# Optimization experiments

Hardware: AMD Instinct MI355X
Metric: run time of the kernel (lower is better)

Reference implementation:

```python
import jax, jax.numpy as jnp
import numpy as np

N, E, G = 50000, 800000, 64
IN, HID, HEADS, OUT = 128, 64, 4, 128
NEG = 0.2  # PyG GATConv default negative_slope


def setup_inputs() -> dict:
    key = jax.random.key(0)
    ks = jax.random.split(key, 12)
    nrm = lambda k, shape, s: (jax.random.normal(k, shape, jnp.float32) * s)
    x = nrm(ks[0], (N, IN), 1.0)
    edge_index = jax.random.randint(ks[1], (2, E), 0, N)
    batch = jnp.sort(jax.random.randint(ks[2], (N,), 0, G))
    W1 = nrm(ks[3], (IN, HEADS * HID), IN ** -0.5)
    a1_src = nrm(ks[4], (HEADS, HID), HID ** -0.5)
    a1_dst = nrm(ks[5], (HEADS, HID), HID ** -0.5)
    b1 = jnp.zeros((HEADS * HID,), jnp.float32)
    W2 = nrm(ks[6], (HEADS * HID, OUT), (HEADS * HID) ** -0.5)
    a2_src = nrm(ks[7], (1, OUT), OUT ** -0.5)
    a2_dst = nrm(ks[8], (1, OUT), OUT ** -0.5)
    b2 = jnp.zeros((OUT,), jnp.float32)
    fc_W = nrm(ks[9], (OUT, OUT), OUT ** -0.5)
    fc_b = jnp.zeros((OUT,), jnp.float32)
    return dict(x=x, edge_index=edge_index, batch=batch, W1=W1, a1_src=a1_src,
                a1_dst=a1_dst, b1=b1, W2=W2, a2_src=a2_src, a2_dst=a2_dst,
                b2=b2, fc_W=fc_W, fc_b=fc_b)


def gat_conv(x, W, a_src, a_dst, b, src, dst, heads):
    n = x.shape[0]
    ch = W.shape[1] // heads
    h = (x @ W).reshape(n, heads, ch)                      # [n, H, C]
    al_s = jnp.einsum('nhc,hc->nh', h, a_src)              # per-node src logits
    al_d = jnp.einsum('nhc,hc->nh', h, a_dst)
    e = al_s[src] + al_d[dst]                              # [E, H]
    e = jnp.where(e > 0, e, NEG * e)                       # LeakyReLU
    # segment softmax over incoming edges of each dst node
    m = jax.lax.stop_gradient(jax.ops.segment_max(e, dst, num_segments=n))
    m = jnp.where(jnp.isfinite(m), m, 0.0)
    ex = jnp.exp(e - m[dst])
    s = jax.ops.segment_sum(ex, dst, num_segments=n)
    alpha = ex / (s[dst] + 1e-16)                          # [E, H]
    out = jax.ops.segment_sum(h[src] * alpha[..., None], dst, num_segments=n)
    return out.reshape(n, heads * ch) + b                  # concat heads + bias


def reference(x, edge_index, batch, W1, a1_src, a1_dst, b1, W2, a2_src, a2_dst, b2, fc_W, fc_b):
    loops = jnp.arange(N, dtype=edge_index.dtype)          # PyG adds self-loops
    src = jnp.concatenate([edge_index[0], loops])
    dst = jnp.concatenate([edge_index[1], loops])
    h = jax.nn.elu(gat_conv(x, W1, a1_src, a1_dst, b1, src, dst, HEADS))
    h = jax.nn.elu(gat_conv(h, W2, a2_src, a2_dst, b2, src, dst, 1))
    sums = jax.ops.segment_sum(h, batch, num_segments=G)
    cnt = jax.ops.segment_sum(jnp.ones((N,), h.dtype), batch, num_segments=G)
    pooled = sums / jnp.maximum(cnt, 1.0)[:, None]         # global mean pool
    return jax.nn.relu(pooled @ fc_W + fc_b)
```

## Files before the change

kernel.cpp:

```cpp
#include <hip/hip_runtime.h>
#include <math.h>

#define N_NODES 50000
#define N_EDGES 800000
#define N_GRAPHS 64
#define NEG 0.2f
#define CTS 132

typedef unsigned short us;
typedef us us2 __attribute__((ext_vector_type(2)));
typedef us us4 __attribute__((ext_vector_type(4)));
typedef us us8 __attribute__((ext_vector_type(8)));
typedef short bf16x8 __attribute__((ext_vector_type(8)));
typedef float f32x4 __attribute__((ext_vector_type(4)));

__device__ __forceinline__ us bf16rn(float f) {
  unsigned int u = __float_as_uint(f);
  u += 0x7FFFu + ((u >> 16) & 1u);
  return (us)(u >> 16);
}
__device__ __forceinline__ float bf2f(us h) {
  return __uint_as_float(((unsigned int)h) << 16);
}
__device__ __forceinline__ float readlane_f(float v, int l) {
  return __uint_as_float((unsigned)__builtin_amdgcn_readlane(__float_as_uint(v), l));
}

__global__ __launch_bounds__(256) void prep_kernel(
    const float* __restrict__ x, us* __restrict__ xh, us* __restrict__ xl,
    const float* __restrict__ W1, const float* __restrict__ W2,
    us* __restrict__ w1h, us* __restrict__ w1l,
    us* __restrict__ w2h, us* __restrict__ w2l,
    int* __restrict__ cnt, float* __restrict__ psum) {
  int bid = blockIdx.x, t = threadIdx.x;
  if (bid < 6250) {
    int i = bid * 256 + t;
    float4 v = *(const float4*)&x[(size_t)i * 4];
    us h0 = bf16rn(v.x), h1 = bf16rn(v.y), h2 = bf16rn(v.z), h3 = bf16rn(v.w);
    us4 hv = {h0, h1, h2, h3};
    us4 lv = {bf16rn(v.x - bf2f(h0)), bf16rn(v.y - bf2f(h1)),
              bf16rn(v.z - bf2f(h2)), bf16rn(v.w - bf2f(h3))};
    *(us4*)&xh[(size_t)i * 4] = hv;
    *(us4*)&xl[(size_t)i * 4] = lv;
  } else if (bid < 6506) {
    int idx = (bid - 6250) * 256 + t;
    const float* W; us *oh, *ol; int K, N, li;
    if (idx < 128 * 256) { W = W1; oh = w1h; ol = w1l; K = 128; N = 256; li = idx; }
    else { W = W2; oh = w2h; ol = w2l; K = 256; N = 128; li = idx - 128 * 256; }
    int n = li / K, k = li - n * K;
    float f = W[(size_t)k * N + n];
    us h = bf16rn(f);
    oh[li] = h;
    ol[li] = bf16rn(f - bf2f(h));
  } else {
    int i = (bid - 6506) * 256 + t;
    if (i < N_NODES) cnt[i] = 0;
    if (i < N_GRAPHS * 128) psum[i] = 0.f;
  }
}

__global__ __launch_bounds__(256, 2) void gemm_bf16x3(
    const us* __restrict__ Agh, const us* __restrict__ Agl,
    const us* __restrict__ Bth, const us* __restrict__ Btl,
    us* __restrict__ C, int M, int N, int K, int heads,
    const float* __restrict__ a_src, const float* __restrict__ a_dst,
    float* __restrict__ al_s, float* __restrict__ al_d) {
  __shared__ us smem[4][128][40];
  int t = threadIdx.x;
  int m0 = blockIdx.x * 128;
  int n0 = blockIdx.y * 128;
  int w = t >> 6, l = t & 63;
  int wr = w >> 1, wc = w & 1;
  int l15 = l & 15, g = l >> 4;

  f32x4 acc[4][4] = {};

  for (int kb = 0; kb < K; kb += 32) {
    us8 z = {};
    #pragma unroll
    for (int i = 0; i < 2; i++) {
      int slot = i * 256 + t;
      int row = slot >> 2, kq = slot & 3;
      size_t gi = (size_t)(m0 + row) * K + kb + kq * 8;
      bool ok = (m0 + row) < M;
      *(us8*)&smem[0][row][kq * 8] = ok ? *(const us8*)&Agh[gi] : z;
      *(us8*)&smem[1][row][kq * 8] = ok ? *(const us8*)&Agl[gi] : z;
    }
    #pragma unroll
    for (int i = 0; i < 2; i++) {
      int slot = i * 256 + t;
      int n = slot >> 2, kq = slot & 3;
      size_t gi = (size_t)(n0 + n) * K + kb + kq * 8;
      *(us8*)&smem[2][n][kq * 8] = *(const us8*)&Bth[gi];
      *(us8*)&smem[3][n][kq * 8] = *(const us8*)&Btl[gi];
    }
    __syncthreads();

    bf16x8 af[4], al4[4], bf[4], bl4[4];
    #pragma unroll
    for (int i = 0; i < 4; i++) {
      af[i]  = *(const bf16x8*)&smem[0][wr * 64 + i * 16 + l15][g * 8];
      al4[i] = *(const bf16x8*)&smem[1][wr * 64 + i * 16 + l15][g * 8];
      bf[i]  = *(const bf16x8*)&smem[2][wc * 64 + i * 16 + l15][g * 8];
      bl4[i] = *(const bf16x8*)&smem[3][wc * 64 + i * 16 + l15][g * 8];
    }
    #pragma unroll
    for (int i = 0; i < 4; i++)
      #pragma unroll
      for (int j = 0; j < 4; j++) {
        acc[i][j] = __builtin_amdgcn_mfma_f32_16x16x32_bf16(af[i], bf[j], acc[i][j], 0, 0, 0);
        acc[i][j] = __builtin_amdgcn_mfma_f32_16x16x32_bf16(af[i], bl4[j], acc[i][j], 0, 0, 0);
        acc[i][j] = __builtin_amdgcn_mfma_f32_16x16x32_bf16(al4[i], bf[j], acc[i][j], 0, 0, 0);
      }
    __syncthreads();
  }

  us* ct = &smem[0][0][0];
  #pragma unroll
  for (int i = 0; i < 4; i++)
    #pragma unroll
    for (int j = 0; j < 4; j++)
      #pragma unroll
      for (int r = 0; r < 4; r++) {
        int row = wr * 64 + i * 16 + g * 4 + r;
        int col = wc * 64 + j * 16 + l15;
        ct[row * CTS + col] = bf16rn(acc[i][j][r]);
      }
  __syncthreads();
  #pragma unroll
  for (int q = 0; q < 8; q++) {
    int slot = q * 256 + t;
    int row = slot >> 4, col8 = slot & 15;
    if (m0 + row < M) {
      us8 v = *(const us8*)&ct[row * CTS + col8 * 8];
      *(us8*)&C[(size_t)(m0 + row) * N + n0 + col8 * 8] = v;
    }
  }

  if (heads == 4) {
    int r = t & 127, hs = t >> 7;
    int row = m0 + r;
    if (row < M) {
      int head = blockIdx.y * 2 + hs;
      const float* as = &a_src[head * 64];
      const float* ad = &a_dst[head * 64];
      float ss = 0.f, sd = 0.f;
      #pragma unroll
      for (int k8 = 0; k8 < 8; k8++) {
        us8 v = *(const us8*)&ct[r * CTS + hs * 64 + k8 * 8];
        #pragma unroll
        for (int j = 0; j < 8; j++) {
          float f = bf2f(v[j]);
          ss += f * as[k8 * 8 + j];
          sd += f * ad[k8 * 8 + j];
        }
      }
      al_s[row * 4 + head] = ss;
      al_d[row * 4 + head] = sd;
    }
  } else if (heads == 1) {
    if (t < 128) {
      int row = m0 + t;
      if (row < M) {
        float ss = 0.f, sd = 0.f;
        #pragma unroll
        for (int k8 = 0; k8 < 16; k8++) {
          us8 v = *(const us8*)&ct[t * CTS + k8 * 8];
          #pragma unroll
          for (int j = 0; j < 8; j++) {
            float f = bf2f(v[j]);
            ss += f * a_src[k8 * 8 + j];
            sd += f * a_dst[k8 * 8 + j];
          }
        }
        al_s[row] = ss;
        al_d[row] = sd;
      }
    }
  }
}

__global__ __launch_bounds__(256) void count_kernel(const int* __restrict__ dst,
                                                    int* __restrict__ cnt) {
  int e = blockIdx.x * 256 + threadIdx.x;
  if (e < N_EDGES) atomicAdd(&cnt[dst[e]], 1);
}

__global__ __launch_bounds__(256) void scan1_kernel(const int* __restrict__ cnt,
                                                    int* __restrict__ itmp,
                                                    int* __restrict__ bsum) {
  int i = blockIdx.x * 256 + threadIdx.x;
  int v = (i < N_NODES) ? cnt[i] : 0;
  int lane = threadIdx.x & 63, w = threadIdx.x >> 6;
  int s = v;
  #pragma unroll
  for (int off = 1; off < 64; off <<= 1) {
    int tv = __shfl_up(s, off);
    if (lane >= off) s += tv;
  }
  __shared__ int wsum[4];
  if (lane == 63) wsum[w] = s;
  __syncthreads();
  int add = 0;
  for (int p = 0; p < w; p++) add += wsum[p];
  s += add;
  if (i < N_NODES) itmp[i] = s;
  if (threadIdx.x == 255) bsum[blockIdx.x] = s;
}

__global__ __launch_bounds__(256) void scan3_kernel(const int* __restrict__ cnt,
                                                    const int* __restrict__ itmp,
                                                    const int* __restrict__ bsum,
                                                    int* __restrict__ rowst,
                                                    int* __restrict__ cursor,
                                                    int nb) {
  int t = threadIdx.x;
  int lane = t & 63, w = t >> 6;
  int v = (t < nb && t < blockIdx.x) ? bsum[t] : 0;
  int s = v;
  #pragma unroll
  for (int off = 1; off < 64; off <<= 1) s += __shfl_xor(s, off);
  __shared__ int partial[4];
  if (lane == 0) partial[w] = s;
  __syncthreads();
  int boff = partial[0] + partial[1] + partial[2] + partial[3];
  int i = blockIdx.x * 256 + t;
  if (i < N_NODES) {
    int excl = itmp[i] - cnt[i] + boff;
    rowst[i] = excl;
    cursor[i] = excl;
  }
  if (i == 0) rowst[N_NODES] = N_EDGES;
}

__global__ __launch_bounds__(256) void scatter_kernel(
    const int* __restrict__ src, const int* __restrict__ dst,
    int* __restrict__ cursor, int* __restrict__ csr_src) {
  int e = blockIdx.x * 256 + threadIdx.x;
  if (e < N_EDGES) {
    int p = atomicAdd(&cursor[dst[e]], 1);
    csr_src[p] = src[e];
  }
}

__global__ __launch_bounds__(256) void agg1_kernel(
    const us* __restrict__ h1b, const float* __restrict__ al_s,
    const float* __restrict__ al_d, const int* __restrict__ rowst,
    const int* __restrict__ csrc, const float* __restrict__ b1,
    us* __restrict__ outh, us* __restrict__ outl) {
  int d = (blockIdx.x * 256 + threadIdx.x) >> 6;
  int lane = threadIdx.x & 63;
  if (d >= N_NODES) return;
  int head = lane >> 4;
  int c0 = lane * 4;
  int wsel = lane & 48;
  float ald = al_d[d * 4 + head];
  float wsum = 0.f, a0 = 0.f, a1 = 0.f, a2 = 0.f, a3 = 0.f;
  {
    float v = al_s[d * 4 + head] + ald;
    v = v > 0.f ? v : NEG * v;
    float w = __expf(v);
    us4 hv = *(const us4*)&h1b[(size_t)d * 256 + c0];
    wsum += w;
    a0 += w * bf2f(hv[0]); a1 += w * bf2f(hv[1]);
    a2 += w * bf2f(hv[2]); a3 += w * bf2f(hv[3]);
  }
  int beg = rowst[d], end = rowst[d + 1];
  int j = beg;
  for (; j + 16 <= end; j += 16) {
    int el = lane & 15;
    int sv = csrc[j + el];
    float v = al_s[sv * 4 + head] + ald;
    v = v > 0.f ? v : NEG * v;
    float wv = __expf(v);
    #pragma unroll
    for (int q = 0; q < 16; q += 4) {
      int s0 = __builtin_amdgcn_readlane(sv, q + 0);
      int s1 = __builtin_amdgcn_readlane(sv, q + 1);
      int s2 = __builtin_amdgcn_readlane(sv, q + 2);
      int s3 = __builtin_amdgcn_readlane(sv, q + 3);
      us4 h0 = *(const us4*)&h1b[(size_t)(unsigned)s0 * 256 + c0];
      us4 h1 = *(const us4*)&h1b[(size_t)(unsigned)s1 * 256 + c0];
      us4 h2 = *(const us4*)&h1b[(size_t)(unsigned)s2 * 256 + c0];
      us4 h3 = *(const us4*)&h1b[(size_t)(unsigned)s3 * 256 + c0];
      float w0 = __shfl(wv, q + 0 + wsel);
      float w1 = __shfl(wv, q + 1 + wsel);
      float w2 = __shfl(wv, q + 2 + wsel);
      float w3 = __shfl(wv, q + 3 + wsel);
      wsum += w0 + w1 + w2 + w3;
      a0 += w0 * bf2f(h0[0]) + w1 * bf2f(h1[0]) + w2 * bf2f(h2[0]) + w3 * bf2f(h3[0]);
      a1 += w0 * bf2f(h0[1]) + w1 * bf2f(h1[1]) + w2 * bf2f(h2[1]) + w3 * bf2f(h3[1]);
      a2 += w0 * bf2f(h0[2]) + w1 * bf2f(h1[2]) + w2 * bf2f(h2[2]) + w3 * bf2f(h3[2]);
      a3 += w0 * bf2f(h0[3]) + w1 * bf2f(h1[3]) + w2 * bf2f(h2[3]) + w3 * bf2f(h3[3]);
    }
  }
  int m = end - j;
  if (m > 0) {
    int el = lane & 15;
    int sv = csrc[j + (el < m ? el : 0)];
    float v = al_s[sv * 4 + head] + ald;
    v = v > 0.f ? v : NEG * v;
    float wv = __expf(v);
    for (int q = 0; q < m; q += 4) {
      int k0 = q, k1 = q + 1 < m ? q + 1 : 0, k2 = q + 2 < m ? q + 2 : 0,
          k3 = q + 3 < m ? q + 3 : 0;
      int s0 = __builtin_amdgcn_readlane(sv, k0);
      int s1 = __builtin_amdgcn_readlane(sv, k1);
      int s2 = __builtin_amdgcn_readlane(sv, k2);
      int s3 = __builtin_amdgcn_readlane(sv, k3);
      us4 h0 = *(const us4*)&h1b[(size_t)(unsigned)s0 * 256 + c0];
      us4 h1 = *(const us4*)&h1b[(size_t)(unsigned)s1 * 256 + c0];
      us4 h2 = *(const us4*)&h1b[(size_t)(unsigned)s2 * 256 + c0];
      us4 h3 = *(const us4*)&h1b[(size_t)(unsigned)s3 * 256 + c0];
      float w0 = __shfl(wv, k0 + wsel);
      float w1 = __shfl(wv, k1 + wsel);
      float w2 = __shfl(wv, k2 + wsel);
      float w3 = __shfl(wv, k3 + wsel);
      if (q + 1 >= m) w1 = 0.f;
      if (q + 2 >= m) w2 = 0.f;
      if (q + 3 >= m) w3 = 0.f;
      wsum += w0 + w1 + w2 + w3;
      a0 += w0 * bf2f(h0[0]) + w1 * bf2f(h1[0]) + w2 * bf2f(h2[0]) + w3 * bf2f(h3[0]);
      a1 += w0 * bf2f(h0[1]) + w1 * bf2f(h1[1]) + w2 * bf2f(h2[1]) + w3 * bf2f(h3[1]);
      a2 += w0 * bf2f(h0[2]) + w1 * bf2f(h1[2]) + w2 * bf2f(h2[2]) + w3 * bf2f(h3[2]);
      a3 += w0 * bf2f(h0[3]) + w1 * bf2f(h1[3]) + w2 * bf2f(h2[3]) + w3 * bf2f(h3[3]);
    }
  }
  float inv = 1.f / (wsum + 1e-16f);
  float4 bb = *(const float4*)&b1[c0];
  float o[4] = {a0 * inv + bb.x, a1 * inv + bb.y, a2 * inv + bb.z, a3 * inv + bb.w};
  us4 oh, ol;
  #pragma unroll
  for (int i = 0; i < 4; i++) {
    float e = o[i] > 0.f ? o[i] : expm1f(o[i]);
    us h = bf16rn(e);
    oh[i] = h;
    ol[i] = bf16rn(e - bf2f(h));
  }
  *(us4*)&outh[(size_t)d * 256 + c0] = oh;
  *(us4*)&outl[(size_t)d * 256 + c0] = ol;
}

__global__ __launch_bounds__(256) void agg2_kernel(
    const us* __restrict__ h2b, const float* __restrict__ al_s,
    const float* __restrict__ al_d, const int* __restrict__ rowst,
    const int* __restrict__ csrc, const float* __restrict__ b2,
    float* __restrict__ out) {
  int d = (blockIdx.x * 256 + threadIdx.x) >> 6;
  int lane = threadIdx.x & 63;
  if (d >= N_NODES) return;
  int c0 = lane * 2;
  float ald = al_d[d];
  float wsum = 0.f, a0 = 0.f, a1 = 0.f;
  {
    float v = al_s[d] + ald;
    v = v > 0.f ? v : NEG * v;
    float w = __expf(v);
    us2 hv = *(const us2*)&h2b[(size_t)d * 128 + c0];
    wsum += w;
    a0 += w * bf2f(hv[0]); a1 += w * bf2f(hv[1]);
  }
  int beg = rowst[d], end = rowst[d + 1];
  int j = beg;
  for (; j + 64 <= end; j += 64) {
    int sv = csrc[j + lane];
    float v = al_s[sv] + ald;
    v = v > 0.f ? v : NEG * v;
    float wvv = __expf(v);
    for (int q = 0; q < 64; q += 4) {
      int s0 = __builtin_amdgcn_readlane(sv, q + 0);
      int s1 = __builtin_amdgcn_readlane(sv, q + 1);
      int s2 = __builtin_amdgcn_readlane(sv, q + 2);
      int s3 = __builtin_amdgcn_readlane(sv, q + 3);
      us2 h0 = *(const us2*)&h2b[(size_t)(unsigned)s0 * 128 + c0];
      us2 h1 = *(const us2*)&h2b[(size_t)(unsigned)s1 * 128 + c0];
      us2 h2 = *(const us2*)&h2b[(size_t)(unsigned)s2 * 128 + c0];
      us2 h3 = *(const us2*)&h2b[(size_t)(unsigned)s3 * 128 + c0];
      float w0 = readlane_f(wvv, q + 0);
      float w1 = readlane_f(wvv, q + 1);
      float w2 = readlane_f(wvv, q + 2);
      float w3 = readlane_f(wvv, q + 3);
      wsum += w0 + w1 + w2 + w3;
      a0 += w0 * bf2f(h0[0]) + w1 * bf2f(h1[0]) + w2 * bf2f(h2[0]) + w3 * bf2f(h3[0]);
      a1 += w0 * bf2f(h0[1]) + w1 * bf2f(h1[1]) + w2 * bf2f(h2[1]) + w3 * bf2f(h3[1]);
    }
  }
  int m = end - j;
  if (m > 0) {
    int sv = csrc[j + (lane < m ? lane : 0)];
    float v = al_s[sv] + ald;
    v = v > 0.f ? v : NEG * v;
    float wvv = __expf(v);
    for (int q = 0; q < m; q += 4) {
      int k0 = q, k1 = q + 1 < m ? q + 1 : 0, k2 = q + 2 < m ? q + 2 : 0,
          k3 = q + 3 < m ? q + 3 : 0;
      int s0 = __builtin_amdgcn_readlane(sv, k0);
      int s1 = __builtin_amdgcn_readlane(sv, k1);
      int s2 = __builtin_amdgcn_readlane(sv, k2);
      int s3 = __builtin_amdgcn_readlane(sv, k3);
      us2 h0 = *(const us2*)&h2b[(size_t)(unsigned)s0 * 128 + c0];
      us2 h1 = *(const us2*)&h2b[(size_t)(unsigned)s1 * 128 + c0];
      us2 h2 = *(const us2*)&h2b[(size_t)(unsigned)s2 * 128 + c0];
      us2 h3 = *(const us2*)&h2b[(size_t)(unsigned)s3 * 128 + c0];
      float w0 = readlane_f(wvv, k0);
      float w1 = readlane_f(wvv, k1);
      float w2 = readlane_f(wvv, k2);
      float w3 = readlane_f(wvv, k3);
      if (q + 1 >= m) w1 = 0.f;
      if (q + 2 >= m) w2 = 0.f;
      if (q + 3 >= m) w3 = 0.f;
      wsum += w0 + w1 + w2 + w3;
      a0 += w0 * bf2f(h0[0]) + w1 * bf2f(h1[0]) + w2 * bf2f(h2[0]) + w3 * bf2f(h3[0]);
      a1 += w0 * bf2f(h0[1]) + w1 * bf2f(h1[1]) + w2 * bf2f(h2[1]) + w3 * bf2f(h3[1]);
    }
  }
  float inv = 1.f / (wsum + 1e-16f);
  float2 bb = *(const float2*)&b2[c0];
  float o0 = a0 * inv + bb.x, o1 = a1 * inv + bb.y;
  o0 = o0 > 0.f ? o0 : expm1f(o0);
  o1 = o1 > 0.f ? o1 : expm1f(o1);
  *(float2*)&out[(size_t)d * 128 + c0] = make_float2(o0, o1);
}

#define PNPB 128
__global__ __launch_bounds__(256) void pool_kernel(const float* __restrict__ y,
                                                   const int* __restrict__ batch,
                                                   float* __restrict__ psum) {
  int t = threadIdx.x;
  int lane32 = t & 31;
  int sub = t >> 5;
  int base = blockIdx.x * PNPB + sub * (PNPB / 8);
  int nend = base + PNPB / 8;
  if (nend > N_NODES) nend = N_NODES;
  float4 acc = make_float4(0.f, 0.f, 0.f, 0.f);
  int curg = -1;
  for (int n = base; n < nend; ++n) {
    int g = batch[n];
    if (g != curg) {
      if (curg >= 0) {
        float* p = &psum[curg * 128 + lane32 * 4];
        atomicAdd(p + 0, acc.x); atomicAdd(p + 1, acc.y);
        atomicAdd(p + 2, acc.z); atomicAdd(p + 3, acc.w);
      }
      acc = make_float4(0.f, 0.f, 0.f, 0.f);
      curg = g;
    }
    float4 v = *(const float4*)&y[(size_t)n * 128 + lane32 * 4];
    acc.x += v.x; acc.y += v.y; acc.z += v.z; acc.w += v.w;
  }
  if (curg >= 0) {
    float* p = &psum[curg * 128 + lane32 * 4];
    atomicAdd(p + 0, acc.x); atomicAdd(p + 1, acc.y);
    atomicAdd(p + 2, acc.z); atomicAdd(p + 3, acc.w);
  }
}

__global__ __launch_bounds__(128) void fc_kernel(
    const float* __restrict__ psum, const int* __restrict__ batch,
    const float* __restrict__ fcW, const float* __restrict__ fcb,
    float* __restrict__ out) {
  __shared__ float pr[128];
  __shared__ int bounds[2];
  int g = blockIdx.x, c = threadIdx.x;
  if (c < 2) {
    int target = g + c;
    int lo = 0, hi = N_NODES;
    while (lo < hi) {
      int mid = (lo + hi) >> 1;
      if (batch[mid] < target) lo = mid + 1; else hi = mid;
    }
    bounds[c] = lo;
  }
  __syncthreads();
  float cnt = (float)(bounds[1] - bounds[0]);
  cnt = cnt > 1.f ? cnt : 1.f;
  pr[c] = psum[g * 128 + c] / cnt;
  __syncthreads();
  float s = fcb[c];
  #pragma unroll 8
  for (int k = 0; k < 128; k++) s += pr[k] * fcW[k * 128 + c];
  out[g * 128 + c] = fmaxf(s, 0.f);
}

extern "C" void kernel_launch(void* const* d_in, const int* in_sizes, int n_in,
                              void* d_out, int out_size, void* d_ws,
                              size_t ws_size, hipStream_t stream) {
  const float* x      = (const float*)d_in[0];
  const int*   ei     = (const int*)d_in[1];
  const int*   batch  = (const int*)d_in[2];
  const float* W1     = (const float*)d_in[3];
  const float* a1_src = (const float*)d_in[4];
  const float* a1_dst = (const float*)d_in[5];
  const float* b1     = (const float*)d_in[6];
  const float* W2     = (const float*)d_in[7];
  const float* a2_src = (const float*)d_in[8];
  const float* a2_dst = (const float*)d_in[9];
  const float* b2     = (const float*)d_in[10];
  const float* fc_W   = (const float*)d_in[11];
  const float* fc_b   = (const float*)d_in[12];
  float* out = (float*)d_out;

  const int* srcp = ei;
  const int* dstp = ei + N_EDGES;
  const int NB = (N_NODES + 255) / 256;

  float* y    = (float*)d_ws;
  float* al1s = y + (size_t)N_NODES * 128;
  float* al1d = al1s + N_NODES * 4;
  float* al2s = al1d + N_NODES * 4;
  float* al2d = al2s + N_NODES;
  float* psum = al2d + N_NODES;
  us* xh   = (us*)(psum + N_GRAPHS * 128);
  us* xl   = xh + (size_t)N_NODES * 128;
  us* x2h  = xl + (size_t)N_NODES * 128;
  us* x2l  = x2h + (size_t)N_NODES * 256;
  us* h1b  = x2l + (size_t)N_NODES * 256;
  us* h2b  = h1b + (size_t)N_NODES * 256;
  us* w1th = h2b + (size_t)N_NODES * 128;
  us* w1tl = w1th + 256 * 128;
  us* w2th = w1tl + 256 * 128;
  us* w2tl = w2th + 128 * 256;
  int* cnt    = (int*)(w2tl + 128 * 256);
  int* bsum   = cnt + N_NODES;
  int* itmp   = bsum + 256;
  int* rowst  = itmp + N_NODES;
  int* cursor = rowst + N_NODES + 8;
  int* csrc   = cursor + N_NODES;
  size_t needed = (size_t)((char*)(csrc + N_EDGES) - (char*)d_ws);
  if (ws_size < needed) return;

  prep_kernel<<<6702, 256, 0, stream>>>(x, xh, xl, W1, W2, w1th, w1tl, w2th,
                                        w2tl, cnt, psum);

  count_kernel<<<(N_EDGES + 255) / 256, 256, 0, stream>>>(dstp, cnt);
  scan1_kernel<<<NB, 256, 0, stream>>>(cnt, itmp, bsum);
  scan3_kernel<<<NB, 256, 0, stream>>>(cnt, itmp, bsum, rowst, cursor, NB);
  scatter_kernel<<<(N_EDGES + 255) / 256, 256, 0, stream>>>(srcp, dstp, cursor, csrc);

  gemm_bf16x3<<<dim3(391, 2), 256, 0, stream>>>(xh, xl, w1th, w1tl, h1b,
                                                N_NODES, 256, 128, 4, a1_src,
                                                a1_dst, al1s, al1d);
  agg1_kernel<<<(N_NODES * 64 + 255) / 256, 256, 0, stream>>>(
      h1b, al1s, al1d, rowst, csrc, b1, x2h, x2l);

  gemm_bf16x3<<<dim3(391, 1), 256, 0, stream>>>(x2h, x2l, w2th, w2tl, h2b,
                                                N_NODES, 128, 256, 1, a2_src,
                                                a2_dst, al2s, al2d);
  agg2_kernel<<<(N_NODES * 64 + 255) / 256, 256, 0, stream>>>(
      h2b, al2s, al2d, rowst, csrc, b2, y);

  pool_kernel<<<(N_NODES + PNPB - 1) / PNPB, 256, 0, stream>>>(y, batch, psum);
  fc_kernel<<<N_GRAPHS, 128, 0, stream>>>(psum, batch, fc_W, fc_b, out);
}
```

Before: 283.4 us.

## Fuse edge counting into prep kernel and widen agg2 gathers to 8-byte loads

```diff
diff --git a/kernel.cpp b/kernel.cpp
--- a/kernel.cpp
+++ b/kernel.cpp
@@ -31,7 +31,7 @@
     const float* __restrict__ W1, const float* __restrict__ W2,
     us* __restrict__ w1h, us* __restrict__ w1l,
     us* __restrict__ w2h, us* __restrict__ w2l,
-    int* __restrict__ cnt, float* __restrict__ psum) {
+    const int* __restrict__ dst, int* __restrict__ cnt) {
   int bid = blockIdx.x, t = threadIdx.x;
   if (bid < 6250) {
     int i = bid * 256 + t;
@@ -53,9 +53,8 @@
     oh[li] = h;
     ol[li] = bf16rn(f - bf2f(h));
   } else {
-    int i = (bid - 6506) * 256 + t;
-    if (i < N_NODES) cnt[i] = 0;
-    if (i < N_GRAPHS * 128) psum[i] = 0.f;
+    int e = (bid - 6506) * 256 + t;
+    if (e < N_EDGES) atomicAdd(&cnt[dst[e]], 1);
   }
 }
 
@@ -178,12 +177,6 @@
       }
     }
   }
-}
-
-__global__ __launch_bounds__(256) void count_kernel(const int* __restrict__ dst,
-                                                    int* __restrict__ cnt) {
-  int e = blockIdx.x * 256 + threadIdx.x;
-  if (e < N_EDGES) atomicAdd(&cnt[dst[e]], 1);
 }
 
 __global__ __launch_bounds__(256) void scan1_kernel(const int* __restrict__ cnt,
@@ -349,16 +342,18 @@
   int d = (blockIdx.x * 256 + threadIdx.x) >> 6;
   int lane = threadIdx.x & 63;
   if (d >= N_NODES) return;
-  int c0 = lane * 2;
+  int half = lane >> 5;
+  int c0 = (lane & 31) * 4;
   float ald = al_d[d];
-  float wsum = 0.f, a0 = 0.f, a1 = 0.f;
+  float wsum = 0.f, a0 = 0.f, a1 = 0.f, a2 = 0.f, a3 = 0.f;
   {
     float v = al_s[d] + ald;
     v = v > 0.f ? v : NEG * v;
-    float w = __expf(v);
-    us2 hv = *(const us2*)&h2b[(size_t)d * 128 + c0];
+    float w = half ? 0.f : __expf(v);
+    us4 hv = *(const us4*)&h2b[(size_t)d * 128 + c0];
     wsum += w;
     a0 += w * bf2f(hv[0]); a1 += w * bf2f(hv[1]);
+    a2 += w * bf2f(hv[2]); a3 += w * bf2f(hv[3]);
   }
   int beg = rowst[d], end = rowst[d + 1];
   int j = beg;
@@ -366,23 +361,22 @@
     int sv = csrc[j + lane];
     float v = al_s[sv] + ald;
     v = v > 0.f ? v : NEG * v;
-    float wvv = __expf(v);
-    for (int q = 0; q < 64; q += 4) {
-      int s0 = __builtin_amdgcn_readlane(sv, q + 0);
-      int s1 = __builtin_amdgcn_readlane(sv, q + 1);
-      int s2 = __builtin_amdgcn_readlane(sv, q + 2);
-      int s3 = __builtin_amdgcn_readlane(sv, q + 3);
-      us2 h0 = *(const us2*)&h2b[(size_t)(unsigned)s0 * 128 + c0];
-      us2 h1 = *(const us2*)&h2b[(size_t)(unsigned)s1 * 128 + c0];
-      us2 h2 = *(const us2*)&h2b[(size_t)(unsigned)s2 * 128 + c0];
-      us2 h3 = *(const us2*)&h2b[(size_t)(unsigned)s3 * 128 + c0];
-      float w0 = readlane_f(wvv, q + 0);
-      float w1 = readlane_f(wvv, q + 1);
-      float w2 = readlane_f(wvv, q + 2);
-      float w3 = readlane_f(wvv, q + 3);
+    float wv = __expf(v);
+    for (int p = 0; p < 64; p += 8) {
+      int e0 = p + 0 + half, e1 = p + 2 + half, e2 = p + 4 + half, e3 = p + 6 + half;
+      int s0 = __shfl(sv, e0), s1 = __shfl(sv, e1);
+      int s2 = __shfl(sv, e2), s3 = __shfl(sv, e3);
+      us4 h0 = *(const us4*)&h2b[(size_t)(unsigned)s0 * 128 + c0];
+      us4 h1 = *(const us4*)&h2b[(size_t)(unsigned)s1 * 128 + c0];
+      us4 h2v = *(const us4*)&h2b[(size_t)(unsigned)s2 * 128 + c0];
+      us4 h3 = *(const us4*)&h2b[(size_t)(unsigned)s3 * 128 + c0];
+      float w0 = __shfl(wv, e0), w1 = __shfl(wv, e1);
+      float w2 = __shfl(wv, e2), w3 = __shfl(wv, e3);
       wsum += w0 + w1 + w2 + w3;
-      a0 += w0 * bf2f(h0[0]) + w1 * bf2f(h1[0]) + w2 * bf2f(h2[0]) + w3 * bf2f(h3[0]);
-      a1 += w0 * bf2f(h0[1]) + w1 * bf2f(h1[1]) + w2 * bf2f(h2[1]) + w3 * bf2f(h3[1]);
+      a0 += w0 * bf2f(h0[0]) + w1 * bf2f(h1[0]) + w2 * bf2f(h2v[0]) + w3 * bf2f(h3[0]);
+      a1 += w0 * bf2f(h0[1]) + w1 * bf2f(h1[1]) + w2 * bf2f(h2v[1]) + w3 * bf2f(h3[1]);
+      a2 += w0 * bf2f(h0[2]) + w1 * bf2f(h1[2]) + w2 * bf2f(h2v[2]) + w3 * bf2f(h3[2]);
+      a3 += w0 * bf2f(h0[3]) + w1 * bf2f(h1[3]) + w2 * bf2f(h2v[3]) + w3 * bf2f(h3[3]);
     }
   }
   int m = end - j;
@@ -390,36 +384,46 @@
     int sv = csrc[j + (lane < m ? lane : 0)];
     float v = al_s[sv] + ald;
     v = v > 0.f ? v : NEG * v;
-    float wvv = __expf(v);
-    for (int q = 0; q < m; q += 4) {
-      int k0 = q, k1 = q + 1 < m ? q + 1 : 0, k2 = q + 2 < m ? q + 2 : 0,
-          k3 = q + 3 < m ? q + 3 : 0;
-      int s0 = __builtin_amdgcn_readlane(sv, k0);
-      int s1 = __builtin_amdgcn_readlane(sv, k1);
-      int s2 = __builtin_amdgcn_readlane(sv, k2);
-      int s3 = __builtin_amdgcn_readlane(sv, k3);
-      us2 h0 = *(const us2*)&h2b[(size_t)(unsigned)s0 * 128 + c0];
-      us2 h1 = *(const us2*)&h2b[(size_t)(unsigned)s1 * 128 + c0];
-      us2 h2 = *(const us2*)&h2b[(size_t)(unsigned)s2 * 128 + c0];
-      us2 h3 = *(const us2*)&h2b[(size_t)(unsigned)s3 * 128 + c0];
-      float w0 = readlane_f(wvv, k0);
-      float w1 = readlane_f(wvv, k1);
-      float w2 = readlane_f(wvv, k2);
-      float w3 = readlane_f(wvv, k3);
-      if (q + 1 >= m) w1 = 0.f;
-      if (q + 2 >= m) w2 = 0.f;
-      if (q + 3 >= m) w3 = 0.f;
+    float wv = __expf(v);
+    for (int p = 0; p < m; p += 8) {
+      int e0 = p + 0 + half, e1 = p + 2 + half, e2 = p + 4 + half, e3 = p + 6 + half;
+      int k0 = e0 < m ? e0 : 0, k1 = e1 < m ? e1 : 0;
+      int k2 = e2 < m ? e2 : 0, k3 = e3 < m ? e3 : 0;
+      int s0 = __shfl(sv, k0), s1 = __shfl(sv, k1);
+      int s2 = __shfl(sv, k2), s3 = __shfl(sv, k3);
+      us4 h0 = *(const us4*)&h2b[(size_t)(unsigned)s0 * 128 + c0];
+      us4 h1 = *(const us4*)&h2b[(size_t)(unsigned)s1 * 128 + c0];
+      us4 h2v = *(const us4*)&h2b[(size_t)(unsigned)s2 * 128 + c0];
+      us4 h3 = *(const us4*)&h2b[(size_t)(unsigned)s3 * 128 + c0];
+      float w0 = __shfl(wv, k0), w1 = __shfl(wv, k1);
+      float w2 = __shfl(wv, k2), w3 = __shfl(wv, k3);
+      if (e0 >= m) w0 = 0.f;
+      if (e1 >= m) w1 = 0.f;
+      if (e2 >= m) w2 = 0.f;
+      if (e3 >= m) w3 = 0.f;
       wsum += w0 + w1 + w2 + w3;
-      a0 += w0 * bf2f(h0[0]) + w1 * bf2f(h1[0]) + w2 * bf2f(h2[0]) + w3 * bf2f(h3[0]);
-      a1 += w0 * bf2f(h0[1]) + w1 * bf2f(h1[1]) + w2 * bf2f(h2[1]) + w3 * bf2f(h3[1]);
-    }
-  }
-  float inv = 1.f / (wsum + 1e-16f);
-  float2 bb = *(const float2*)&b2[c0];
-  float o0 = a0 * inv + bb.x, o1 = a1 * inv + bb.y;
-  o0 = o0 > 0.f ? o0 : expm1f(o0);
-  o1 = o1 > 0.f ? o1 : expm1f(o1);
-  *(float2*)&out[(size_t)d * 128 + c0] = make_float2(o0, o1);
+      a0 += w0 * bf2f(h0[0]) + w1 * bf2f(h1[0]) + w2 * bf2f(h2v[0]) + w3 * bf2f(h3[0]);
+      a1 += w0 * bf2f(h0[1]) + w1 * bf2f(h1[1]) + w2 * bf2f(h2v[1]) + w3 * bf2f(h3[1]);
+      a2 += w0 * bf2f(h0[2]) + w1 * bf2f(h1[2]) + w2 * bf2f(h2v[2]) + w3 * bf2f(h3[2]);
+      a3 += w0 * bf2f(h0[3]) + w1 * bf2f(h1[3]) + w2 * bf2f(h2v[3]) + w3 * bf2f(h3[3]);
+    }
+  }
+  wsum += __shfl_xor(wsum, 32);
+  a0 += __shfl_xor(a0, 32);
+  a1 += __shfl_xor(a1, 32);
+  a2 += __shfl_xor(a2, 32);
+  a3 += __shfl_xor(a3, 32);
+  if (half == 0) {
+    float inv = 1.f / (wsum + 1e-16f);
+    float4 bb = *(const float4*)&b2[c0];
+    float o0 = a0 * inv + bb.x, o1 = a1 * inv + bb.y;
+    float o2 = a2 * inv + bb.z, o3 = a3 * inv + bb.w;
+    o0 = o0 > 0.f ? o0 : expm1f(o0);
+    o1 = o1 > 0.f ? o1 : expm1f(o1);
+    o2 = o2 > 0.f ? o2 : expm1f(o2);
+    o3 = o3 > 0.f ? o3 : expm1f(o3);
+    *(float4*)&out[(size_t)d * 128 + c0] = make_float4(o0, o1, o2, o3);
+  }
 }
 
 #define PNPB 128
@@ -529,10 +533,12 @@
   size_t needed = (size_t)((char*)(csrc + N_EDGES) - (char*)d_ws);
   if (ws_size < needed) return;
 
-  prep_kernel<<<6702, 256, 0, stream>>>(x, xh, xl, W1, W2, w1th, w1tl, w2th,
-                                        w2tl, cnt, psum);
-
-  count_kernel<<<(N_EDGES + 255) / 256, 256, 0, stream>>>(dstp, cnt);
+  hipMemsetAsync(cnt, 0, N_NODES * sizeof(int), stream);
+  hipMemsetAsync(psum, 0, N_GRAPHS * 128 * sizeof(float), stream);
+
+  prep_kernel<<<9631, 256, 0, stream>>>(x, xh, xl, W1, W2, w1th, w1tl, w2th,
+                                        w2tl, dstp, cnt);
+
   scan1_kernel<<<NB, 256, 0, stream>>>(cnt, itmp, bsum);
   scan3_kernel<<<NB, 256, 0, stream>>>(cnt, itmp, bsum, rowst, cursor, NB);
   scatter_kernel<<<(N_EDGES + 255) / 256, 256, 0, stream>>>(srcp, dstp, cursor, csrc);
```

New measurement: 288.4 us. About the same (+1.8%).
